# Performance work log

Measured on AMD Instinct MI355X. Metric: run time of the kernel, lower is better.

## Reference

```python
import jax, jax.numpy as jnp
import numpy as np

N = 50000      # nodes
E = 200000     # edges
S = 8          # edge feature dim
F_IN = 32      # node feature dim after GraphMasking
F = 32         # ECCConv channels
G = 512        # graphs in disjoint batch
P = 1024       # preference pairs
N_OUT = 1      # config['n_out']


def _ecc(x, e, src, tgt, Wk, bk, root, b):
    # edge-conditioned filters: [E, F_in, F_out]
    kern = (e @ Wk + bk).reshape(E, x.shape[1], -1)
    # gather source node feats, apply per-edge filter, scatter-sum to targets
    msgs = jnp.einsum('ei,eio->eo', x[src], kern)
    agg = jax.ops.segment_sum(msgs, tgt, num_segments=N)
    return jax.nn.relu(agg + x @ root + b)


def setup_inputs() -> dict:
    key = jax.random.key(0)
    ks = jax.random.split(key, 12)
    s = 0.1
    return {
        'x': jax.random.normal(ks[0], (N, F_IN + 1), jnp.float32),
        'e': jax.random.normal(ks[1], (E, S), jnp.float32),
        'sources': jax.random.randint(ks[2], (E,), 0, N),
        'targets': jax.random.randint(ks[3], (E,), 0, N),
        'seg': jnp.sort(jax.random.randint(ks[4], (N,), 0, G)),
        'idx_a': jax.random.randint(ks[5], (P,), 0, G),
        'idx_b': jax.random.randint(ks[6], (P,), 0, G),
        'Wk1': jax.random.normal(ks[7], (S, F_IN * F), jnp.float32) * s,
        'bk1': jnp.zeros((F_IN * F,), jnp.float32),
        'root1': jax.random.normal(ks[8], (F_IN, F), jnp.float32) * s,
        'b1': jnp.zeros((F,), jnp.float32),
        'Wk2': jax.random.normal(ks[9], (S, F * F), jnp.float32) * s,
        'bk2': jnp.zeros((F * F,), jnp.float32),
        'root2': jax.random.normal(ks[10], (F, F), jnp.float32) * s,
        'b2': jnp.zeros((F,), jnp.float32),
        'Wd': jax.random.normal(ks[11], (F, N_OUT), jnp.float32) * s,
        'bd': jnp.zeros((N_OUT,), jnp.float32),
    }


def reference(x, e, sources, targets, seg, idx_a, idx_b,
              Wk1, bk1, root1, b1, Wk2, bk2, root2, b2, Wd, bd):
    h = x[:, :-1]                         # GraphMasking: drop mask column
    h = _ecc(h, e, sources, targets, Wk1, bk1, root1, b1)
    h = _ecc(h, e, sources, targets, Wk2, bk2, root2, b2)
    # tf.cast(x, int32): truncation (exact for nonneg relu output),
    # non-differentiable like the original cast.
    h = jax.lax.stop_gradient(jnp.trunc(h))
    pooled = jax.ops.segment_sum(h, seg, num_segments=G)   # GlobalSumPool
    out = jax.nn.relu(pooled @ Wd + bd)                    # Dense(n_out, relu)
    return out[idx_b] - out[idx_a]                         # pref lookup diff
```

## Files before the change

### kernel.cpp

```cpp
#include <hip/hip_runtime.h>

#define N_NODES 50000
#define N_EDGES 200000
#define S_DIM   8
#define F_DIM   32
#define G_SEG   512
#define P_PAIRS 1024
#define A_COLS  288
#define SCAN_B  196
#define NB      16

__global__ __launch_bounds__(256)
void zero_init(int* __restrict__ deg, float* __restrict__ pooled)
{
    const int gid = blockIdx.x * 256 + threadIdx.x;
    if (gid < N_NODES) deg[gid] = 0;
    if (gid < G_SEG * F_DIM) pooled[gid] = 0.f;
}

__global__ __launch_bounds__(256)
void deg_hist(const int* __restrict__ src, int* __restrict__ deg)
{
    const int e = blockIdx.x * 256 + threadIdx.x;
    if (e < N_EDGES) atomicAdd(&deg[src[e]], 1);
}

__global__ __launch_bounds__(256)
void sum_blocks(const int* __restrict__ deg, int* __restrict__ partial)
{
    __shared__ int sd[256];
    const int t = threadIdx.x;
    const int n = blockIdx.x * 256 + t;
    sd[t] = (n < N_NODES) ? deg[n] : 0;
    __syncthreads();
    for (int off = 128; off > 0; off >>= 1) {
        if (t < off) sd[t] += sd[t + off];
        __syncthreads();
    }
    if (t == 0) partial[blockIdx.x] = sd[0];
}

__global__ __launch_bounds__(256)
void scan_partials(const int* __restrict__ partial, int* __restrict__ blockoff)
{
    __shared__ int sd[256];
    const int t = threadIdx.x;
    sd[t] = (t < SCAN_B) ? partial[t] : 0;
    __syncthreads();
    for (int off = 1; off < 256; off <<= 1) {
        int v = (t >= off) ? sd[t - off] : 0;
        __syncthreads();
        sd[t] += v;
        __syncthreads();
    }
    if (t < SCAN_B) blockoff[t] = (t == 0) ? 0 : sd[t - 1];
}

__global__ __launch_bounds__(256)
void write_rowstart(const int* __restrict__ deg, const int* __restrict__ blockoff,
                    int* __restrict__ rowstart, int* __restrict__ cursor)
{
    __shared__ int sd[256];
    const int t = threadIdx.x;
    const int n = blockIdx.x * 256 + t;
    const int d = (n < N_NODES) ? deg[n] : 0;
    sd[t] = d;
    __syncthreads();
    for (int off = 1; off < 256; off <<= 1) {
        int v = (t >= off) ? sd[t - off] : 0;
        __syncthreads();
        sd[t] += v;
        __syncthreads();
    }
    if (n < N_NODES) {
        const int rs = blockoff[blockIdx.x] + sd[t] - d;
        rowstart[n] = rs;
        cursor[n]   = rs;
    }
    if (blockIdx.x == 0 && t == 0) rowstart[N_NODES] = N_EDGES;
}

__global__ __launch_bounds__(256)
void csr_scatter(const int* __restrict__ src, const int* __restrict__ tgt,
                 const float* __restrict__ evec, int* __restrict__ cursor,
                 int* __restrict__ srcs, int* __restrict__ tgts,
                 float* __restrict__ esort)
{
    const int e = blockIdx.x * 256 + threadIdx.x;
    if (e < N_EDGES) {
        const int sn  = src[e];
        const int pos = atomicAdd(&cursor[sn], 1);
        srcs[pos] = sn;
        tgts[pos] = tgt[e];
        const float4* s4 = (const float4*)(evec + (size_t)e * S_DIM);
        float4* d4 = (float4*)(esort + (size_t)pos * S_DIM);
        d4[0] = s4[0];
        d4[1] = s4[1];
    }
}

template <int LAYER>
__global__ __launch_bounds__(256)
void agg_init(const float* __restrict__ hsrc, const float* __restrict__ root,
              const float* __restrict__ bias, float* __restrict__ agg)
{
    __shared__ float r[F_DIM * F_DIM];
    __shared__ float bsh[F_DIM];
    for (int t = threadIdx.x; t < F_DIM * F_DIM; t += 256) r[t] = root[t];
    if (threadIdx.x < F_DIM) bsh[threadIdx.x] = bias[threadIdx.x];
    __syncthreads();

    const int gid = blockIdx.x * 256 + threadIdx.x;
    if (gid >= N_NODES * F_DIM) return;
    const int n = gid >> 5, o = gid & 31;

    float acc = bsh[o];
    #pragma unroll
    for (int i = 0; i < F_DIM; ++i) {
        float h;
        if (LAYER == 0) h = hsrc[(size_t)n * (F_DIM + 1) + i];
        else {
            h = hsrc[(size_t)n * F_DIM + i];
            h = h > 0.f ? h : 0.f;
        }
        acc += h * r[i * F_DIM + o];
    }
    agg[gid] = acc;
}

template <int LAYER>
__global__ __launch_bounds__(320)
void fused_ecc(const float* __restrict__ hsrc,
               const float* __restrict__ Wk, const float* __restrict__ bk,
               const int* __restrict__ rowstart, const int* __restrict__ srcs,
               const int* __restrict__ tgts, const float* __restrict__ esort,
               float* __restrict__ agg)
{
    __shared__ float hh[NB][F_DIM];
    __shared__ float At[NB][A_COLS];

    const int nb   = blockIdx.x * NB;
    const int nmax = (N_NODES - nb < NB) ? (N_NODES - nb) : NB;

    if (LAYER == 0) {
        for (int idx = threadIdx.x; idx < nmax * F_DIM; idx += 320) {
            const int n = idx >> 5, i = idx & 31;
            hh[n][i] = hsrc[(size_t)(nb + n) * (F_DIM + 1) + i];
        }
    } else {
        const float4* s4 = (const float4*)(hsrc + (size_t)nb * F_DIM);
        for (int idx = threadIdx.x; idx < nmax * (F_DIM / 4); idx += 320) {
            float4 v = s4[idx];
            v.x = v.x > 0.f ? v.x : 0.f;
            v.y = v.y > 0.f ? v.y : 0.f;
            v.z = v.z > 0.f ? v.z : 0.f;
            v.w = v.w > 0.f ? v.w : 0.f;
            ((float4*)hh)[idx] = v;
        }
    }
    __syncthreads();

    const int c = threadIdx.x;
    if (c < A_COLS) {
        float w[F_DIM];
        const int o = c & 31;
        if (c < 256) {
            const int s = c >> 5;
            #pragma unroll
            for (int i = 0; i < F_DIM; ++i) w[i] = Wk[s * (F_DIM * F_DIM) + i * F_DIM + o];
        } else {
            #pragma unroll
            for (int i = 0; i < F_DIM; ++i) w[i] = bk[i * F_DIM + o];
        }
        for (int n = 0; n < nmax; ++n) {
            const float4* hv = (const float4*)hh[n];
            float acc = 0.f;
            #pragma unroll
            for (int i4 = 0; i4 < F_DIM / 4; ++i4) {
                float4 h4 = hv[i4];
                acc += h4.x * w[4*i4]   + h4.y * w[4*i4+1]
                     + h4.z * w[4*i4+2] + h4.w * w[4*i4+3];
            }
            At[n][c] = acc;
        }
    }
    __syncthreads();

    const int r0 = rowstart[nb];
    const int r1 = rowstart[nb + nmax];
    const int nwork = (r1 - r0) * F_DIM;
    for (int idx = threadIdx.x; idx < nwork; idx += 320) {
        const int pos = r0 + (idx >> 5);
        const int o   = idx & 31;
        const int ls  = srcs[pos] - nb;
        const int tn  = tgts[pos];
        const float4* ev4 = (const float4*)(esort + (size_t)pos * S_DIM);
        const float4 e0 = ev4[0];
        const float4 e1 = ev4[1];
        const float* Ar = At[ls];
        float m = Ar[8 * F_DIM + o];
        m += e0.x * Ar[0 * F_DIM + o];
        m += e0.y * Ar[1 * F_DIM + o];
        m += e0.z * Ar[2 * F_DIM + o];
        m += e0.w * Ar[3 * F_DIM + o];
        m += e1.x * Ar[4 * F_DIM + o];
        m += e1.y * Ar[5 * F_DIM + o];
        m += e1.z * Ar[6 * F_DIM + o];
        m += e1.w * Ar[7 * F_DIM + o];
        atomicAdd(&agg[(size_t)tn * F_DIM + o], m);
    }
}

__global__ __launch_bounds__(256)
void pool_kernel(const float* __restrict__ agg2, const int* __restrict__ seg,
                 float* __restrict__ pooled)
{
    const int o    = threadIdx.x & 31;
    const int r    = threadIdx.x >> 5;
    const int base = blockIdx.x * 256 + r * 32;

    int   curseg = -1;
    float acc    = 0.f;
    for (int i = 0; i < 32; ++i) {
        const int n = base + i;
        if (n >= N_NODES) break;
        const int sg = seg[n];
        if (sg != curseg) {
            if (curseg >= 0 && acc != 0.f)
                atomicAdd(&pooled[(size_t)curseg * F_DIM + o], acc);
            curseg = sg;
            acc = 0.f;
        }
        float v = agg2[(size_t)n * F_DIM + o];
        v = v > 0.f ? v : 0.f;
        acc += truncf(v);
    }
    if (curseg >= 0 && acc != 0.f)
        atomicAdd(&pooled[(size_t)curseg * F_DIM + o], acc);
}

__global__ __launch_bounds__(512)
void head_kernel(const float* __restrict__ pooled, const float* __restrict__ Wd,
                 const float* __restrict__ bd, const int* __restrict__ ia,
                 const int* __restrict__ ib, float* __restrict__ out)
{
    __shared__ float og[G_SEG];
    const int g = threadIdx.x;
    if (g < G_SEG) {
        float acc = bd[0];
        #pragma unroll
        for (int i = 0; i < F_DIM; ++i) acc += pooled[(size_t)g * F_DIM + i] * Wd[i];
        og[g] = acc > 0.f ? acc : 0.f;
    }
    __syncthreads();
    for (int p = threadIdx.x; p < P_PAIRS; p += 512)
        out[p] = og[ib[p]] - og[ia[p]];
}

extern "C" void kernel_launch(void* const* d_in, const int* in_sizes, int n_in,
                              void* d_out, int out_size, void* d_ws, size_t ws_size,
                              hipStream_t stream)
{
    const float* x    = (const float*)d_in[0];
    const float* e    = (const float*)d_in[1];
    const int*   src  = (const int*)d_in[2];
    const int*   tgt  = (const int*)d_in[3];
    const int*   seg  = (const int*)d_in[4];
    const int*   ia   = (const int*)d_in[5];
    const int*   ib   = (const int*)d_in[6];
    const float* Wk1  = (const float*)d_in[7];
    const float* bk1  = (const float*)d_in[8];
    const float* root1= (const float*)d_in[9];
    const float* b1   = (const float*)d_in[10];
    const float* Wk2  = (const float*)d_in[11];
    const float* bk2  = (const float*)d_in[12];
    const float* root2= (const float*)d_in[13];
    const float* b2   = (const float*)d_in[14];
    const float* Wd   = (const float*)d_in[15];
    const float* bd   = (const float*)d_in[16];
    float* out = (float*)d_out;

    float* ag1    = (float*)d_ws;
    float* ag2    = ag1 + (size_t)N_NODES * F_DIM;
    float* pooled = ag2 + (size_t)N_NODES * F_DIM;
    float* esort  = pooled + (size_t)G_SEG * F_DIM;
    int*   deg      = (int*)(esort + (size_t)N_EDGES * S_DIM);
    int*   cursor   = deg + N_NODES;
    int*   rowstart = cursor + N_NODES;
    int*   partial  = rowstart + (N_NODES + 1);
    int*   blockoff = partial + SCAN_B;
    int*   srcs     = blockoff + SCAN_B;
    int*   tgts     = srcs + N_EDGES;

    const int eblk = (N_EDGES + 255) / 256;
    const int fblk = (N_NODES + NB - 1) / NB;
    const int iblk = (N_NODES * F_DIM + 255) / 256;

    zero_init     <<<SCAN_B, 256, 0, stream>>>(deg, pooled);
    deg_hist      <<<eblk, 256, 0, stream>>>(src, deg);
    sum_blocks    <<<SCAN_B, 256, 0, stream>>>(deg, partial);
    scan_partials <<<1, 256, 0, stream>>>(partial, blockoff);
    write_rowstart<<<SCAN_B, 256, 0, stream>>>(deg, blockoff, rowstart, cursor);
    csr_scatter   <<<eblk, 256, 0, stream>>>(src, tgt, e, cursor, srcs, tgts, esort);

    agg_init<0><<<iblk, 256, 0, stream>>>(x, root1, b1, ag1);
    fused_ecc<0><<<fblk, 320, 0, stream>>>(x,   Wk1, bk1, rowstart, srcs, tgts, esort, ag1);
    agg_init<1><<<iblk, 256, 0, stream>>>(ag1, root2, b2, ag2);
    fused_ecc<1><<<fblk, 320, 0, stream>>>(ag1, Wk2, bk2, rowstart, srcs, tgts, esort, ag2);

    pool_kernel<<<SCAN_B, 256, 0, stream>>>(ag2, seg, pooled);
    head_kernel<<<1, 512, 0, stream>>>(pooled, Wd, bd, ia, ib, out);
}
```

Measured before the change: 201.3 us.

## Replace float atomic scatter with target-sorted message buffer and segmented reduce

```diff
diff --git a/kernel.cpp b/kernel.cpp
--- a/kernel.cpp
+++ b/kernel.cpp
@@ -7,31 +7,37 @@
 #define G_SEG   512
 #define P_PAIRS 1024
 #define A_COLS  288
+#define NB      16
+#define N2      (2 * N_NODES)
+#define SCAN_B2 391
 #define SCAN_B  196
-#define NB      16
-
-__global__ __launch_bounds__(256)
-void zero_init(int* __restrict__ deg, float* __restrict__ pooled)
+
+__global__ __launch_bounds__(256)
+void zero_init(int* __restrict__ deg2, float* __restrict__ pooled)
 {
     const int gid = blockIdx.x * 256 + threadIdx.x;
-    if (gid < N_NODES) deg[gid] = 0;
+    if (gid < N2) deg2[gid] = 0;
     if (gid < G_SEG * F_DIM) pooled[gid] = 0.f;
 }
 
 __global__ __launch_bounds__(256)
-void deg_hist(const int* __restrict__ src, int* __restrict__ deg)
+void deg_hist(const int* __restrict__ src, const int* __restrict__ tgt,
+              int* __restrict__ deg2)
 {
     const int e = blockIdx.x * 256 + threadIdx.x;
-    if (e < N_EDGES) atomicAdd(&deg[src[e]], 1);
-}
-
-__global__ __launch_bounds__(256)
-void sum_blocks(const int* __restrict__ deg, int* __restrict__ partial)
+    if (e < N_EDGES) {
+        atomicAdd(&deg2[src[e]], 1);
+        atomicAdd(&deg2[N_NODES + tgt[e]], 1);
+    }
+}
+
+__global__ __launch_bounds__(256)
+void sum_blocks(const int* __restrict__ deg2, int* __restrict__ partial)
 {
     __shared__ int sd[256];
     const int t = threadIdx.x;
     const int n = blockIdx.x * 256 + t;
-    sd[t] = (n < N_NODES) ? deg[n] : 0;
+    sd[t] = (n < N2) ? deg2[n] : 0;
     __syncthreads();
     for (int off = 128; off > 0; off >>= 1) {
         if (t < off) sd[t] += sd[t + off];
@@ -40,30 +46,30 @@
     if (t == 0) partial[blockIdx.x] = sd[0];
 }
 
-__global__ __launch_bounds__(256)
+__global__ __launch_bounds__(512)
 void scan_partials(const int* __restrict__ partial, int* __restrict__ blockoff)
 {
-    __shared__ int sd[256];
+    __shared__ int sd[512];
     const int t = threadIdx.x;
-    sd[t] = (t < SCAN_B) ? partial[t] : 0;
-    __syncthreads();
-    for (int off = 1; off < 256; off <<= 1) {
+    sd[t] = (t < SCAN_B2) ? partial[t] : 0;
+    __syncthreads();
+    for (int off = 1; off < 512; off <<= 1) {
         int v = (t >= off) ? sd[t - off] : 0;
         __syncthreads();
         sd[t] += v;
         __syncthreads();
     }
-    if (t < SCAN_B) blockoff[t] = (t == 0) ? 0 : sd[t - 1];
-}
-
-__global__ __launch_bounds__(256)
-void write_rowstart(const int* __restrict__ deg, const int* __restrict__ blockoff,
-                    int* __restrict__ rowstart, int* __restrict__ cursor)
+    if (t < SCAN_B2) blockoff[t] = (t == 0) ? 0 : sd[t - 1];
+}
+
+__global__ __launch_bounds__(256)
+void write_rowstart(const int* __restrict__ deg2, const int* __restrict__ blockoff,
+                    int* __restrict__ row, int* __restrict__ cursor)
 {
     __shared__ int sd[256];
     const int t = threadIdx.x;
     const int n = blockIdx.x * 256 + t;
-    const int d = (n < N_NODES) ? deg[n] : 0;
+    const int d = (n < N2) ? deg2[n] : 0;
     sd[t] = d;
     __syncthreads();
     for (int off = 1; off < 256; off <<= 1) {
@@ -72,26 +78,28 @@
         sd[t] += v;
         __syncthreads();
     }
-    if (n < N_NODES) {
+    if (n < N2) {
         const int rs = blockoff[blockIdx.x] + sd[t] - d;
-        rowstart[n] = rs;
-        cursor[n]   = rs;
-    }
-    if (blockIdx.x == 0 && t == 0) rowstart[N_NODES] = N_EDGES;
+        row[n]    = rs;
+        cursor[n] = rs;
+    }
+    if (blockIdx.x == 0 && t == 0) row[N2] = 2 * N_EDGES;
 }
 
 __global__ __launch_bounds__(256)
 void csr_scatter(const int* __restrict__ src, const int* __restrict__ tgt,
                  const float* __restrict__ evec, int* __restrict__ cursor,
-                 int* __restrict__ srcs, int* __restrict__ tgts,
+                 int* __restrict__ srcs, int* __restrict__ postgt,
                  float* __restrict__ esort)
 {
     const int e = blockIdx.x * 256 + threadIdx.x;
     if (e < N_EDGES) {
         const int sn  = src[e];
-        const int pos = atomicAdd(&cursor[sn], 1);
-        srcs[pos] = sn;
-        tgts[pos] = tgt[e];
+        const int tn  = tgt[e];
+        const int pos  = atomicAdd(&cursor[sn], 1);
+        const int post = atomicAdd(&cursor[N_NODES + tn], 1) - N_EDGES;
+        srcs[pos]   = sn;
+        postgt[pos] = post;
         const float4* s4 = (const float4*)(evec + (size_t)e * S_DIM);
         float4* d4 = (float4*)(esort + (size_t)pos * S_DIM);
         d4[0] = s4[0];
@@ -132,9 +140,9 @@
 __global__ __launch_bounds__(320)
 void fused_ecc(const float* __restrict__ hsrc,
                const float* __restrict__ Wk, const float* __restrict__ bk,
-               const int* __restrict__ rowstart, const int* __restrict__ srcs,
-               const int* __restrict__ tgts, const float* __restrict__ esort,
-               float* __restrict__ agg)
+               const int* __restrict__ row, const int* __restrict__ srcs,
+               const int* __restrict__ postgt, const float* __restrict__ esort,
+               float* __restrict__ msgbuf)
 {
     __shared__ float hh[NB][F_DIM];
     __shared__ float At[NB][A_COLS];
@@ -186,14 +194,14 @@
     }
     __syncthreads();
 
-    const int r0 = rowstart[nb];
-    const int r1 = rowstart[nb + nmax];
+    const int r0 = row[nb];
+    const int r1 = row[nb + nmax];
     const int nwork = (r1 - r0) * F_DIM;
     for (int idx = threadIdx.x; idx < nwork; idx += 320) {
         const int pos = r0 + (idx >> 5);
         const int o   = idx & 31;
         const int ls  = srcs[pos] - nb;
-        const int tn  = tgts[pos];
+        const int pt  = postgt[pos];
         const float4* ev4 = (const float4*)(esort + (size_t)pos * S_DIM);
         const float4 e0 = ev4[0];
         const float4 e1 = ev4[1];
@@ -207,8 +215,26 @@
         m += e1.y * Ar[5 * F_DIM + o];
         m += e1.z * Ar[6 * F_DIM + o];
         m += e1.w * Ar[7 * F_DIM + o];
-        atomicAdd(&agg[(size_t)tn * F_DIM + o], m);
-    }
+        msgbuf[(size_t)pt * F_DIM + o] = m;
+    }
+}
+
+__global__ __launch_bounds__(256)
+void seg_reduce(const float* __restrict__ msgbuf, const int* __restrict__ row,
+                float* __restrict__ agg)
+{
+    const int o    = threadIdx.x & 31;
+    const int tloc = threadIdx.x >> 5;
+    const int t    = blockIdx.x * 8 + tloc;
+    if (t >= N_NODES) return;
+
+    const int r0 = row[N_NODES + t] - N_EDGES;
+    const int r1 = row[N_NODES + t + 1] - N_EDGES;
+
+    float acc = agg[(size_t)t * F_DIM + o];
+    for (int r = r0; r < r1; ++r)
+        acc += msgbuf[(size_t)r * F_DIM + o];
+    agg[(size_t)t * F_DIM + o] = acc;
 }
 
 __global__ __launch_bounds__(256)
@@ -284,29 +310,34 @@
     float* ag2    = ag1 + (size_t)N_NODES * F_DIM;
     float* pooled = ag2 + (size_t)N_NODES * F_DIM;
     float* esort  = pooled + (size_t)G_SEG * F_DIM;
-    int*   deg      = (int*)(esort + (size_t)N_EDGES * S_DIM);
-    int*   cursor   = deg + N_NODES;
-    int*   rowstart = cursor + N_NODES;
-    int*   partial  = rowstart + (N_NODES + 1);
-    int*   blockoff = partial + SCAN_B;
-    int*   srcs     = blockoff + SCAN_B;
-    int*   tgts     = srcs + N_EDGES;
+    float* msgbuf = esort + (size_t)N_EDGES * S_DIM;
+    int*   deg2     = (int*)(msgbuf + (size_t)N_EDGES * F_DIM);
+    int*   cursor   = deg2 + N2;
+    int*   row      = cursor + N2;
+    int*   partial  = row + (N2 + 1);
+    int*   blockoff = partial + SCAN_B2;
+    int*   srcs     = blockoff + SCAN_B2;
+    int*   postgt   = srcs + N_EDGES;
 
     const int eblk = (N_EDGES + 255) / 256;
     const int fblk = (N_NODES + NB - 1) / NB;
     const int iblk = (N_NODES * F_DIM + 255) / 256;
-
-    zero_init     <<<SCAN_B, 256, 0, stream>>>(deg, pooled);
-    deg_hist      <<<eblk, 256, 0, stream>>>(src, deg);
-    sum_blocks    <<<SCAN_B, 256, 0, stream>>>(deg, partial);
-    scan_partials <<<1, 256, 0, stream>>>(partial, blockoff);
-    write_rowstart<<<SCAN_B, 256, 0, stream>>>(deg, blockoff, rowstart, cursor);
-    csr_scatter   <<<eblk, 256, 0, stream>>>(src, tgt, e, cursor, srcs, tgts, esort);
+    const int rblk = (N_NODES + 7) / 8;
+
+    zero_init     <<<SCAN_B2, 256, 0, stream>>>(deg2, pooled);
+    deg_hist      <<<eblk, 256, 0, stream>>>(src, tgt, deg2);
+    sum_blocks    <<<SCAN_B2, 256, 0, stream>>>(deg2, partial);
+    scan_partials <<<1, 512, 0, stream>>>(partial, blockoff);
+    write_rowstart<<<SCAN_B2, 256, 0, stream>>>(deg2, blockoff, row, cursor);
+    csr_scatter   <<<eblk, 256, 0, stream>>>(src, tgt, e, cursor, srcs, postgt, esort);
 
     agg_init<0><<<iblk, 256, 0, stream>>>(x, root1, b1, ag1);
-    fused_ecc<0><<<fblk, 320, 0, stream>>>(x,   Wk1, bk1, rowstart, srcs, tgts, esort, ag1);
+    fused_ecc<0><<<fblk, 320, 0, stream>>>(x, Wk1, bk1, row, srcs, postgt, esort, msgbuf);
+    seg_reduce <<<rblk, 256, 0, stream>>>(msgbuf, row, ag1);
+
     agg_init<1><<<iblk, 256, 0, stream>>>(ag1, root2, b2, ag2);
-    fused_ecc<1><<<fblk, 320, 0, stream>>>(ag1, Wk2, bk2, rowstart, srcs, tgts, esort, ag2);
+    fused_ecc<1><<<fblk, 320, 0, stream>>>(ag1, Wk2, bk2, row, srcs, postgt, esort, msgbuf);
+    seg_reduce <<<rblk, 256, 0, stream>>>(msgbuf, row, ag2);
 
     pool_kernel<<<SCAN_B, 256, 0, stream>>>(ag2, seg, pooled);
     head_kernel<<<1, 512, 0, stream>>>(pooled, Wd, bd, ia, ib, out);
```

Result: slower. 234.0 us (+16.2%).
